# Kernel optimization log

Measured on AMD Instinct MI355X. Metric: run time of the kernel, lower is better.

The kernel has to match this reference:

```python
import jax, jax.numpy as jnp
import numpy as np

NX = 768
N_HEAD = 12
N_CTX = 2048
BATCH = 4
EPS = 1e-5
NEG = -1000000000.0


def _layernorm(x, g, b):
    # NOTE: faithful to source bug: returns g + normalized + b (additive, not scale)
    u = jnp.mean(x, axis=-1, keepdims=True)
    s = jnp.mean((x - u) ** 2, axis=-1, keepdims=True)
    return g + (x - u) / jnp.sqrt(s + EPS) + b


def setup_inputs() -> dict:
    key = jax.random.key(0)
    ks = jax.random.split(key, 8)
    std = 0.02
    x = jax.random.normal(ks[0], (BATCH, N_CTX, NX), dtype=jnp.float32)
    w_attn = jax.random.normal(ks[1], (NX, 3 * NX), dtype=jnp.float32) * std
    b_attn = jnp.zeros((3 * NX,), jnp.float32)
    w_proj = jax.random.normal(ks[2], (NX, NX), dtype=jnp.float32) * std
    b_proj = jnp.zeros((NX,), jnp.float32)
    ln1_g = jnp.ones((NX,), jnp.float32)
    ln1_b = jnp.zeros((NX,), jnp.float32)
    w_fc = jax.random.normal(ks[3], (NX, 4 * NX), dtype=jnp.float32) * std
    b_fc = jnp.zeros((4 * NX,), jnp.float32)
    w_fc2 = jax.random.normal(ks[4], (4 * NX, NX), dtype=jnp.float32) * std
    b_fc2 = jnp.zeros((NX,), jnp.float32)
    ln2_g = jnp.ones((NX,), jnp.float32)
    ln2_b = jnp.zeros((NX,), jnp.float32)
    return dict(x=x, w_attn=w_attn, b_attn=b_attn, w_proj=w_proj, b_proj=b_proj,
                ln1_g=ln1_g, ln1_b=ln1_b, w_fc=w_fc, b_fc=b_fc,
                w_fc2=w_fc2, b_fc2=b_fc2, ln2_g=ln2_g, ln2_b=ln2_b)


def reference(x, w_attn, b_attn, w_proj, b_proj, ln1_g, ln1_b,
              w_fc, b_fc, w_fc2, b_fc2, ln2_g, ln2_b):
    B, S, D = x.shape
    dh = D // N_HEAD
    # --- attention (scale=False: no 1/sqrt(d)) ---
    qkv = x @ w_attn + b_attn                      # [B,S,3D]
    q, k, v = jnp.split(qkv, 3, axis=-1)
    q = q.reshape(B, S, N_HEAD, dh).transpose(0, 2, 1, 3)   # [B,H,S,dh]
    k = k.reshape(B, S, N_HEAD, dh).transpose(0, 2, 3, 1)   # [B,H,dh,S]
    v = v.reshape(B, S, N_HEAD, dh).transpose(0, 2, 1, 3)   # [B,H,S,dh]
    w = jnp.einsum('bhsd,bhdt->bhst', q, k)        # [B,H,S,S]
    mask = jnp.tril(jnp.ones((S, S), x.dtype))[None, None]
    w = w * mask + NEG * (1.0 - mask)
    w = jax.nn.softmax(w, axis=-1)
    a = jnp.einsum('bhst,bhtd->bhsd', w, v)        # [B,H,S,dh]
    a = a.transpose(0, 2, 1, 3).reshape(B, S, D)
    a = a @ w_proj + b_proj
    # dropout layers are identity (eval mode)
    n = _layernorm(x + a, ln1_g, ln1_b)
    # --- MLP (intended ReLU; source's nn.ReLU usage is a bug) ---
    h = jax.nn.relu(n @ w_fc + b_fc)
    m = h @ w_fc2 + b_fc2
    return _layernorm(n + m, ln2_g, ln2_b)
```

## Files before the change

kernel.cpp:

```cpp
#include <hip/hip_runtime.h>
#include <stdint.h>

#define NX 768
#define SEQ 2048
#define NHEAD 12
#define MROWS 8192
#define LN_EPS 1e-5f
#define MASK_NEG -1000000000.0f

typedef __bf16 bf16x8 __attribute__((ext_vector_type(8)));
typedef float f32x4 __attribute__((ext_vector_type(4)));

#define AS3(p)  ((__attribute__((address_space(3))) void*)(p))
#define AS1C(p) ((const __attribute__((address_space(1))) void*)(p))

__device__ __forceinline__ unsigned short f2bf(float f) {
  union { float f; unsigned int u; } v; v.f = f;
  unsigned int r = v.u + 0x7fffu + ((v.u >> 16) & 1u);
  return (unsigned short)(r >> 16);
}
__device__ __forceinline__ unsigned int f2bf_fast_u(float f) {
  union { float f; unsigned int u; } v; v.f = f;
  return (v.u + 0x8000u) >> 16;
}
__device__ __forceinline__ float bf2f(unsigned short u) {
  union { unsigned int u; float f; } v; v.u = ((unsigned int)u) << 16;
  return v.f;
}

__global__ void convert_f32_bf16(const float* __restrict__ in,
                                 unsigned short* __restrict__ out, int n4) {
  int i = blockIdx.x * blockDim.x + threadIdx.x;
  if (i >= n4) return;
  float4 v = ((const float4*)in)[i];
  ushort4 o;
  o.x = f2bf(v.x); o.y = f2bf(v.y); o.z = f2bf(v.z); o.w = f2bf(v.w);
  ((ushort4*)out)[i] = o;
}

__global__ void transpose_w(const float* __restrict__ w,
                            unsigned short* __restrict__ wt, int K, int N) {
  __shared__ float tile[32][33];
  int n0 = blockIdx.x * 32, k0 = blockIdx.y * 32;
  int tx = threadIdx.x, ty = threadIdx.y;
#pragma unroll
  for (int j = 0; j < 4; ++j)
    tile[ty + j * 8][tx] = w[(long)(k0 + ty + j * 8) * N + n0 + tx];
  __syncthreads();
#pragma unroll
  for (int j = 0; j < 4; ++j)
    wt[(long)(n0 + ty + j * 8) * K + k0 + tx] = f2bf(tile[tx][ty + j * 8]);
}

__global__ void transpose_v(const unsigned short* __restrict__ qkv,
                            unsigned short* __restrict__ vt) {
  __shared__ unsigned short tile[64][68];
  int s0 = blockIdx.x * 64;
  int bh = blockIdx.y, b = bh / NHEAD, h = bh % NHEAD;
  int tx = threadIdx.x, ty = threadIdx.y;
  const unsigned short* src = qkv + (long)b * SEQ * 2304 + 1536 + h * 64;
#pragma unroll
  for (int j = 0; j < 4; ++j) {
    int s = ty + j * 16;
    ushort4 vv = *(const ushort4*)(src + (long)(s0 + s) * 2304 + tx * 4);
    *(ushort4*)(&tile[s][tx * 4]) = vv;
  }
  __syncthreads();
  unsigned short* dst = vt + (long)bh * 64 * SEQ + s0;
#pragma unroll
  for (int j = 0; j < 4; ++j) {
    int d = ty + j * 16;
    ushort4 o;
    o.x = tile[tx * 4 + 0][d]; o.y = tile[tx * 4 + 1][d];
    o.z = tile[tx * 4 + 2][d]; o.w = tile[tx * 4 + 3][d];
    *(ushort4*)(dst + (long)d * SEQ + tx * 4) = o;
  }
}

template <int ACT, int BN>
__global__ __launch_bounds__(256) void gemm_bt(const unsigned short* __restrict__ A,
                                               const unsigned short* __restrict__ Bt,
                                               const float* __restrict__ bias,
                                               unsigned short* __restrict__ C,
                                               int Nsz, int K) {
  __shared__ __align__(16) unsigned short smem[128 * 64 + BN * 64];
  unsigned short* As = smem;
  unsigned short* Bs = smem + 128 * 64;
  const int tid = threadIdx.x;
  const int w = tid >> 6, lane = tid & 63;
  const int l15 = lane & 15, quad = lane >> 4;
  constexpr int MT = (BN == 128) ? 4 : 2;
  const int wrow0 = (BN == 128) ? (w >> 1) * 64 : w * 32;
  const int wcol0 = (BN == 128) ? (w & 1) * 64 : 0;
  const long m0 = (long)blockIdx.y * 128;
  const long n0 = (long)blockIdx.x * BN;

  const int srow = tid >> 3;
  const int sg = tid & 7;

  f32x4 acc[MT][4] = {};

  for (int k0 = 0; k0 < K; k0 += 64) {
#pragma unroll
    for (int p = 0; p < 4; ++p) {
      int row = p * 32 + srow;
      int g = sg ^ (row & 7);
      const unsigned short* gA = A + (m0 + row) * (long)K + k0 + g * 8;
      __builtin_amdgcn_global_load_lds(AS1C(gA), AS3(As + p * 2048 + w * 512), 16, 0, 0);
    }
#pragma unroll
    for (int p = 0; p < BN / 32; ++p) {
      int row = p * 32 + srow;
      int g = sg ^ (row & 7);
      const unsigned short* gB = Bt + (n0 + row) * (long)K + k0 + g * 8;
      __builtin_amdgcn_global_load_lds(AS1C(gB), AS3(Bs + p * 2048 + w * 512), 16, 0, 0);
    }
    __syncthreads();

#pragma unroll
    for (int s2 = 0; s2 < 2; ++s2) {
      const int phys = ((s2 * 4 + quad) ^ (l15 & 7)) * 8;
      bf16x8 af[MT], bfr[4];
#pragma unroll
      for (int mt = 0; mt < MT; ++mt)
        af[mt] = *(const bf16x8*)(As + (wrow0 + mt * 16 + l15) * 64 + phys);
#pragma unroll
      for (int nt = 0; nt < 4; ++nt)
        bfr[nt] = *(const bf16x8*)(Bs + (wcol0 + nt * 16 + l15) * 64 + phys);
#pragma unroll
      for (int mt = 0; mt < MT; ++mt)
#pragma unroll
        for (int nt = 0; nt < 4; ++nt)
          acc[mt][nt] = __builtin_amdgcn_mfma_f32_16x16x32_bf16(af[mt], bfr[nt], acc[mt][nt], 0, 0, 0);
    }
    __syncthreads();
  }

  unsigned short* Ew = smem + w * (16 * 72);
  const long gmB = m0 + wrow0;
  const long gnB = n0 + wcol0;
  float bv[4];
#pragma unroll
  for (int nt = 0; nt < 4; ++nt) bv[nt] = bias[gnB + nt * 16 + l15];
  const int prow = lane >> 3, pcol = (lane & 7) * 8;
#pragma unroll
  for (int mt = 0; mt < MT; ++mt) {
#pragma unroll
    for (int nt = 0; nt < 4; ++nt)
#pragma unroll
      for (int r = 0; r < 4; ++r) {
        float v = acc[mt][nt][r] + bv[nt];
        if (ACT == 1) v = fmaxf(v, 0.f);
        Ew[(quad * 4 + r) * 72 + nt * 16 + l15] = f2bf(v);
      }
#pragma unroll
    for (int ps = 0; ps < 2; ++ps) {
      int row = ps * 8 + prow;
      int4 t = *(const int4*)(Ew + row * 72 + pcol);
      *(int4*)(C + (gmB + mt * 16 + row) * (long)Nsz + gnB + pcol) = t;
    }
  }
}

__global__ __launch_bounds__(256) void attn_v4(const unsigned short* __restrict__ qkv,
                                               const unsigned short* __restrict__ vt,
                                               unsigned short* __restrict__ out) {
  const int bx = blockIdx.x;
  const int bh = blockIdx.y;
  const int b = bh / NHEAD, h = bh % NHEAD;
  const int tid = threadIdx.x;
  const int w = tid >> 6, lane = tid & 63, l15 = lane & 15, quad = lane >> 4;

  __shared__ __align__(16) unsigned short Ks[128 * 64];
  __shared__ __align__(16) unsigned short Vs[64 * 128];
  __shared__ __align__(16) unsigned short Ps[4][16 * 128];

  const long rowbase = (long)b * SEQ;
  unsigned short* Pw = &Ps[w][0];
  const unsigned short* vbh = vt + (long)bh * 64 * SEQ;
  const float LOG2E = 1.4426950408889634f;

  const int krow = tid >> 3;
  const int kgo = (((tid & 7) ^ (krow & 7)) * 8);
  const int vd = tid >> 4;
  const int vgo = (((tid & 15) ^ vd) * 8);
  const unsigned short* kbase = qkv + rowbase * 2304L + 768 + h * 64;

  for (int pass = 0; pass < 2; ++pass) {
    const int qt = (pass == 0) ? bx : 31 - bx;
    const int nkeys = (qt + 1) * 64;
    const int qrow = qt * 64 + w * 16 + l15;
    const int qg = qt * 64 + w * 16 + l15;

    bf16x8 qf[2];
#pragma unroll
    for (int s2 = 0; s2 < 2; ++s2) {
      int4 raw = *(const int4*)(qkv + (rowbase + qrow) * 2304L + h * 64 + s2 * 32 + quad * 8);
      const unsigned short* rp = (const unsigned short*)&raw;
#pragma unroll
      for (int j = 0; j < 8; ++j)
        qf[s2][j] = (__bf16)(bf2f(rp[j]) * LOG2E);
    }

    const unsigned short* kp[4];
    const unsigned short* vp[4];
#pragma unroll
    for (int p = 0; p < 4; ++p) {
      kp[p] = kbase + (long)(p * 32 + krow) * 2304 + kgo;
      vp[p] = vbh + (long)(p * 16 + vd) * SEQ + vgo;
    }

    float l_sum = 0.f;
    f32x4 o_acc[4] = {};

    for (int k0 = 0; k0 < nkeys; k0 += 128) {
      __syncthreads();

#pragma unroll
      for (int p = 0; p < 4; ++p) {
        __builtin_amdgcn_global_load_lds(AS1C(kp[p]), AS3(Ks + p * 2048 + w * 512), 16, 0, 0);
        __builtin_amdgcn_global_load_lds(AS1C(vp[p]), AS3(Vs + p * 2048 + w * 512), 16, 0, 0);
        kp[p] += 128 * 2304;
        vp[p] += 128;
      }
      __syncthreads();

      f32x4 st[8];
#pragma unroll
      for (int nt = 0; nt < 8; ++nt) {
        f32x4 z = {};
        st[nt] = z;
        int key = nt * 16 + l15;
#pragma unroll
        for (int s2 = 0; s2 < 2; ++s2) {
          int phys = (s2 * 4 + quad) ^ (key & 7);
          bf16x8 kf = *(const bf16x8*)(Ks + key * 64 + phys * 8);
          st[nt] = __builtin_amdgcn_mfma_f32_16x16x32_bf16(kf, qf[s2], st[nt], 0, 0, 0);
        }
      }

      if (k0 + 128 > qt * 64) {
#pragma unroll
        for (int nt = 0; nt < 8; ++nt) {
          int kg = k0 + nt * 16 + quad * 4;
#pragma unroll
          for (int r = 0; r < 4; ++r)
            if (kg + r > qg) st[nt][r] = MASK_NEG;
        }
      }

      float psum = 0.f;
#pragma unroll
      for (int nt = 0; nt < 8; ++nt)
#pragma unroll
        for (int r = 0; r < 4; ++r) {
          float p = __builtin_amdgcn_exp2f(st[nt][r]);
          st[nt][r] = p;
          psum += p;
        }
      psum += __shfl_xor(psum, 16);
      psum += __shfl_xor(psum, 32);
      l_sum += psum;

#pragma unroll
      for (int nt = 0; nt < 8; ++nt) {
        unsigned int lo = f2bf_fast_u(st[nt][0]) | (f2bf_fast_u(st[nt][1]) << 16);
        unsigned int hi = f2bf_fast_u(st[nt][2]) | (f2bf_fast_u(st[nt][3]) << 16);
        int g16 = (nt * 2 + (quad >> 1)) ^ l15;
        uint2 pv; pv.x = lo; pv.y = hi;
        *(uint2*)(Pw + l15 * 128 + g16 * 8 + (quad & 1) * 4) = pv;
      }

#pragma unroll
      for (int c = 0; c < 4; ++c) {
        bf16x8 pf = *(const bf16x8*)(Pw + l15 * 128 + (((c * 4 + quad) ^ l15) * 8));
#pragma unroll
        for (int ntd = 0; ntd < 4; ++ntd) {
          int d = ntd * 16 + l15;
          int phys = (c * 4 + quad) ^ l15;
          bf16x8 vf = *(const bf16x8*)(Vs + d * 128 + phys * 8);
          o_acc[ntd] = __builtin_amdgcn_mfma_f32_16x16x32_bf16(pf, vf, o_acc[ntd], 0, 0, 0);
        }
      }
    }

#pragma unroll
    for (int r = 0; r < 4; ++r) {
      float lq = __shfl(l_sum, quad * 4 + r);
      float inv = 1.f / lq;
      int q = qt * 64 + w * 16 + quad * 4 + r;
#pragma unroll
      for (int ntd = 0; ntd < 4; ++ntd) {
        int d = ntd * 16 + l15;
        out[(rowbase + q) * (long)NX + h * 64 + d] = f2bf(o_acc[ntd][r] * inv);
      }
    }
  }
}

__global__ __launch_bounds__(256) void add_ln(const float* __restrict__ x_f,
                                              const unsigned short* __restrict__ x_b,
                                              const unsigned short* __restrict__ y_b,
                                              const float* __restrict__ g,
                                              const float* __restrict__ beta,
                                              float* __restrict__ out_f,
                                              unsigned short* __restrict__ out_b) {
  const int row = blockIdx.x, t = threadIdx.x;
  const long base = (long)row * NX;
  float v[3];
#pragma unroll
  for (int j = 0; j < 3; ++j) {
    int i = t + j * 256;
    float a = x_f ? x_f[base + i] : bf2f(x_b[base + i]);
    v[j] = a + bf2f(y_b[base + i]);
  }
  __shared__ float red[4];
  int wv = t >> 6, ln = t & 63;

  float ssum = v[0] + v[1] + v[2];
#pragma unroll
  for (int sh = 32; sh >= 1; sh >>= 1) ssum += __shfl_xor(ssum, sh);
  if (ln == 0) red[wv] = ssum;
  __syncthreads();
  float u = (red[0] + red[1] + red[2] + red[3]) * (1.f / NX);
  __syncthreads();

  float d0 = v[0] - u, d1 = v[1] - u, d2 = v[2] - u;
  float sq = d0 * d0 + d1 * d1 + d2 * d2;
#pragma unroll
  for (int sh = 32; sh >= 1; sh >>= 1) sq += __shfl_xor(sq, sh);
  if (ln == 0) red[wv] = sq;
  __syncthreads();
  float s = (red[0] + red[1] + red[2] + red[3]) * (1.f / NX);
  float rinv = rsqrtf(s + LN_EPS);

  float dd[3] = {d0, d1, d2};
#pragma unroll
  for (int j = 0; j < 3; ++j) {
    int i = t + j * 256;
    float o = g[i] + dd[j] * rinv + beta[i];
    if (out_f) out_f[base + i] = o;
    else out_b[base + i] = f2bf(o);
  }
}

extern "C" void kernel_launch(void* const* d_in, const int* in_sizes, int n_in,
                              void* d_out, int out_size, void* d_ws, size_t ws_size,
                              hipStream_t stream) {
  const float* x      = (const float*)d_in[0];
  const float* w_attn = (const float*)d_in[1];
  const float* b_attn = (const float*)d_in[2];
  const float* w_proj = (const float*)d_in[3];
  const float* b_proj = (const float*)d_in[4];
  const float* ln1_g  = (const float*)d_in[5];
  const float* ln1_b  = (const float*)d_in[6];
  const float* w_fc   = (const float*)d_in[7];
  const float* b_fc   = (const float*)d_in[8];
  const float* w_fc2  = (const float*)d_in[9];
  const float* b_fc2  = (const float*)d_in[10];
  const float* ln2_g  = (const float*)d_in[11];
  const float* ln2_b  = (const float*)d_in[12];
  float* out = (float*)d_out;

  char* ws = (char*)d_ws;
  size_t off = 0;
  auto alloc = [&](size_t bytes) {
    char* p = ws + off;
    off += (bytes + 255) & ~(size_t)255;
    return p;
  };
  unsigned short* xb      = (unsigned short*)alloc((size_t)MROWS * NX * 2);
  unsigned short* wt_attn = (unsigned short*)alloc((size_t)2304 * 768 * 2);
  unsigned short* wt_proj = (unsigned short*)alloc((size_t)768 * 768 * 2);
  unsigned short* wt_fc   = (unsigned short*)alloc((size_t)3072 * 768 * 2);
  unsigned short* wt_fc2  = (unsigned short*)alloc((size_t)768 * 3072 * 2);
  unsigned short* qkv     = (unsigned short*)alloc((size_t)MROWS * 3072 * 2);
  unsigned short* hbuf    = qkv;
  unsigned short* abuf    = (unsigned short*)alloc((size_t)MROWS * NX * 2);
  unsigned short* mbuf    = abuf;
  unsigned short* nbuf    = (unsigned short*)alloc((size_t)MROWS * NX * 2);
  unsigned short* vtb     = nbuf;
  unsigned short* pout    = xb;

  convert_f32_bf16<<<(MROWS * NX / 4 + 255) / 256, 256, 0, stream>>>(x, xb, MROWS * NX / 4);
  transpose_w<<<dim3(2304 / 32, 768 / 32), dim3(32, 8), 0, stream>>>(w_attn, wt_attn, 768, 2304);
  transpose_w<<<dim3(768 / 32, 768 / 32), dim3(32, 8), 0, stream>>>(w_proj, wt_proj, 768, 768);
  transpose_w<<<dim3(3072 / 32, 768 / 32), dim3(32, 8), 0, stream>>>(w_fc, wt_fc, 768, 3072);
  transpose_w<<<dim3(768 / 32, 3072 / 32), dim3(32, 8), 0, stream>>>(w_fc2, wt_fc2, 3072, 768);

  gemm_bt<0, 128><<<dim3(2304 / 128, MROWS / 128), 256, 0, stream>>>(xb, wt_attn, b_attn, qkv, 2304, 768);
  transpose_v<<<dim3(SEQ / 64, 48), dim3(16, 16), 0, stream>>>(qkv, vtb);
  attn_v4<<<dim3(16, 48), 256, 0, stream>>>(qkv, vtb, abuf);
  gemm_bt<0, 64><<<dim3(768 / 64, MROWS / 128), 256, 0, stream>>>(abuf, wt_proj, b_proj, pout, 768, 768);
  add_ln<<<MROWS, 256, 0, stream>>>(x, nullptr, pout, ln1_g, ln1_b, nullptr, nbuf);
  gemm_bt<1, 128><<<dim3(3072 / 128, MROWS / 128), 256, 0, stream>>>(nbuf, wt_fc, b_fc, hbuf, 3072, 768);
  gemm_bt<0, 64><<<dim3(768 / 64, MROWS / 128), 256, 0, stream>>>(hbuf, wt_fc2, b_fc2, mbuf, 768, 3072);
  add_ln<<<MROWS, 256, 0, stream>>>(nullptr, nbuf, mbuf, ln2_g, ln2_b, out, nullptr);
}
```

Before: 407.8 us.

## Double-buffer LDS tiles in GEMM and attention to overlap loads with MFMA

The GEMM kernel now uses two LDS buffers and issues the next K-tile's global_load_lds before computing on the current one, which also drops one barrier per iteration. The attention kernel is reworked to 64-key tiles with double-buffered K/V in LDS, prefetching the next tile while computing. Masking now applies only to the last tile, so masked work is less wasted. The trade is doubled GEMM shared memory, which may reduce occupancy, and twice as many attention iterations each with a barrier.

```diff
diff --git a/kernel.cpp b/kernel.cpp
--- a/kernel.cpp
+++ b/kernel.cpp
@@ -83,9 +83,10 @@
                                                const float* __restrict__ bias,
                                                unsigned short* __restrict__ C,
                                                int Nsz, int K) {
-  __shared__ __align__(16) unsigned short smem[128 * 64 + BN * 64];
-  unsigned short* As = smem;
-  unsigned short* Bs = smem + 128 * 64;
+  constexpr int ABUF = 128 * 64;
+  constexpr int BBUF = BN * 64;
+  constexpr int BUF = ABUF + BBUF;
+  __shared__ __align__(16) unsigned short smem[2 * BUF];
   const int tid = threadIdx.x;
   const int w = tid >> 6, lane = tid & 63;
   const int l15 = lane & 15, quad = lane >> 4;
@@ -98,9 +99,10 @@
   const int srow = tid >> 3;
   const int sg = tid & 7;
 
-  f32x4 acc[MT][4] = {};
-
-  for (int k0 = 0; k0 < K; k0 += 64) {
+  auto stage = [&](int kb) {
+    unsigned short* As = smem + (kb & 1) * BUF;
+    unsigned short* Bs = As + ABUF;
+    const int k0 = kb * 64;
 #pragma unroll
     for (int p = 0; p < 4; ++p) {
       int row = p * 32 + srow;
@@ -115,8 +117,17 @@
       const unsigned short* gB = Bt + (n0 + row) * (long)K + k0 + g * 8;
       __builtin_amdgcn_global_load_lds(AS1C(gB), AS3(Bs + p * 2048 + w * 512), 16, 0, 0);
     }
+  };
+
+  f32x4 acc[MT][4] = {};
+  const int nkb = K / 64;
+
+  stage(0);
+  for (int kb = 0; kb < nkb; ++kb) {
     __syncthreads();
-
+    if (kb + 1 < nkb) stage(kb + 1);
+    const unsigned short* As = smem + (kb & 1) * BUF;
+    const unsigned short* Bs = As + ABUF;
 #pragma unroll
     for (int s2 = 0; s2 < 2; ++s2) {
       const int phys = ((s2 * 4 + quad) ^ (l15 & 7)) * 8;
@@ -133,8 +144,8 @@
         for (int nt = 0; nt < 4; ++nt)
           acc[mt][nt] = __builtin_amdgcn_mfma_f32_16x16x32_bf16(af[mt], bfr[nt], acc[mt][nt], 0, 0, 0);
     }
-    __syncthreads();
-  }
+  }
+  __syncthreads();
 
   unsigned short* Ew = smem + w * (16 * 72);
   const long gmB = m0 + wrow0;
@@ -162,7 +173,7 @@
   }
 }
 
-__global__ __launch_bounds__(256) void attn_v4(const unsigned short* __restrict__ qkv,
+__global__ __launch_bounds__(256) void attn_v5(const unsigned short* __restrict__ qkv,
                                                const unsigned short* __restrict__ vt,
                                                unsigned short* __restrict__ out) {
   const int bx = blockIdx.x;
@@ -171,9 +182,9 @@
   const int tid = threadIdx.x;
   const int w = tid >> 6, lane = tid & 63, l15 = lane & 15, quad = lane >> 4;
 
-  __shared__ __align__(16) unsigned short Ks[128 * 64];
-  __shared__ __align__(16) unsigned short Vs[64 * 128];
-  __shared__ __align__(16) unsigned short Ps[4][16 * 128];
+  __shared__ __align__(16) unsigned short Ks[2][64 * 64];
+  __shared__ __align__(16) unsigned short Vs[2][64 * 64];
+  __shared__ __align__(16) unsigned short Ps[4][16 * 64];
 
   const long rowbase = (long)b * SEQ;
   unsigned short* Pw = &Ps[w][0];
@@ -182,15 +193,13 @@
 
   const int krow = tid >> 3;
   const int kgo = (((tid & 7) ^ (krow & 7)) * 8);
-  const int vd = tid >> 4;
-  const int vgo = (((tid & 15) ^ vd) * 8);
   const unsigned short* kbase = qkv + rowbase * 2304L + 768 + h * 64;
 
   for (int pass = 0; pass < 2; ++pass) {
     const int qt = (pass == 0) ? bx : 31 - bx;
-    const int nkeys = (qt + 1) * 64;
+    const int niter = qt + 1;
     const int qrow = qt * 64 + w * 16 + l15;
-    const int qg = qt * 64 + w * 16 + l15;
+    const int qg = qrow;
 
     bf16x8 qf[2];
 #pragma unroll
@@ -202,47 +211,57 @@
         qf[s2][j] = (__bf16)(bf2f(rp[j]) * LOG2E);
     }
 
-    const unsigned short* kp[4];
-    const unsigned short* vp[4];
-#pragma unroll
-    for (int p = 0; p < 4; ++p) {
+    const unsigned short* kp[2];
+    const unsigned short* vp[2];
+#pragma unroll
+    for (int p = 0; p < 2; ++p) {
       kp[p] = kbase + (long)(p * 32 + krow) * 2304 + kgo;
-      vp[p] = vbh + (long)(p * 16 + vd) * SEQ + vgo;
+      vp[p] = vbh + (long)(p * 32 + krow) * SEQ + kgo;
     }
 
     float l_sum = 0.f;
     f32x4 o_acc[4] = {};
 
-    for (int k0 = 0; k0 < nkeys; k0 += 128) {
+    __syncthreads();
+#pragma unroll
+    for (int p = 0; p < 2; ++p) {
+      __builtin_amdgcn_global_load_lds(AS1C(kp[p]), AS3(&Ks[0][0] + p * 2048 + w * 512), 16, 0, 0);
+      __builtin_amdgcn_global_load_lds(AS1C(vp[p]), AS3(&Vs[0][0] + p * 2048 + w * 512), 16, 0, 0);
+      kp[p] += 64 * 2304;
+      vp[p] += 64;
+    }
+
+    for (int it = 0; it < niter; ++it) {
       __syncthreads();
-
-#pragma unroll
-      for (int p = 0; p < 4; ++p) {
-        __builtin_amdgcn_global_load_lds(AS1C(kp[p]), AS3(Ks + p * 2048 + w * 512), 16, 0, 0);
-        __builtin_amdgcn_global_load_lds(AS1C(vp[p]), AS3(Vs + p * 2048 + w * 512), 16, 0, 0);
-        kp[p] += 128 * 2304;
-        vp[p] += 128;
-      }
-      __syncthreads();
-
-      f32x4 st[8];
-#pragma unroll
-      for (int nt = 0; nt < 8; ++nt) {
-        f32x4 z = {};
-        st[nt] = z;
+      if (it + 1 < niter) {
+        const int nb = (it + 1) & 1;
+#pragma unroll
+        for (int p = 0; p < 2; ++p) {
+          __builtin_amdgcn_global_load_lds(AS1C(kp[p]), AS3(&Ks[nb][0] + p * 2048 + w * 512), 16, 0, 0);
+          __builtin_amdgcn_global_load_lds(AS1C(vp[p]), AS3(&Vs[nb][0] + p * 2048 + w * 512), 16, 0, 0);
+          kp[p] += 64 * 2304;
+          vp[p] += 64;
+        }
+      }
+      const unsigned short* Kc = &Ks[it & 1][0];
+      const unsigned short* Vc = &Vs[it & 1][0];
+
+      f32x4 st[4] = {};
+#pragma unroll
+      for (int nt = 0; nt < 4; ++nt) {
         int key = nt * 16 + l15;
 #pragma unroll
         for (int s2 = 0; s2 < 2; ++s2) {
           int phys = (s2 * 4 + quad) ^ (key & 7);
-          bf16x8 kf = *(const bf16x8*)(Ks + key * 64 + phys * 8);
+          bf16x8 kf = *(const bf16x8*)(Kc + key * 64 + phys * 8);
           st[nt] = __builtin_amdgcn_mfma_f32_16x16x32_bf16(kf, qf[s2], st[nt], 0, 0, 0);
         }
       }
 
-      if (k0 + 128 > qt * 64) {
-#pragma unroll
-        for (int nt = 0; nt < 8; ++nt) {
-          int kg = k0 + nt * 16 + quad * 4;
+      if (it == niter - 1) {
+#pragma unroll
+        for (int nt = 0; nt < 4; ++nt) {
+          int kg = it * 64 + nt * 16 + quad * 4;
 #pragma unroll
           for (int r = 0; r < 4; ++r)
             if (kg + r > qg) st[nt][r] = MASK_NEG;
@@ -251,7 +270,7 @@
 
       float psum = 0.f;
 #pragma unroll
-      for (int nt = 0; nt < 8; ++nt)
+      for (int nt = 0; nt < 4; ++nt)
 #pragma unroll
         for (int r = 0; r < 4; ++r) {
           float p = __builtin_amdgcn_exp2f(st[nt][r]);
@@ -263,22 +282,22 @@
       l_sum += psum;
 
 #pragma unroll
-      for (int nt = 0; nt < 8; ++nt) {
+      for (int nt = 0; nt < 4; ++nt) {
         unsigned int lo = f2bf_fast_u(st[nt][0]) | (f2bf_fast_u(st[nt][1]) << 16);
         unsigned int hi = f2bf_fast_u(st[nt][2]) | (f2bf_fast_u(st[nt][3]) << 16);
-        int g16 = (nt * 2 + (quad >> 1)) ^ l15;
+        int g8 = (nt * 2 + (quad >> 1)) ^ (l15 & 7);
         uint2 pv; pv.x = lo; pv.y = hi;
-        *(uint2*)(Pw + l15 * 128 + g16 * 8 + (quad & 1) * 4) = pv;
-      }
-
-#pragma unroll
-      for (int c = 0; c < 4; ++c) {
-        bf16x8 pf = *(const bf16x8*)(Pw + l15 * 128 + (((c * 4 + quad) ^ l15) * 8));
+        *(uint2*)(Pw + l15 * 64 + g8 * 8 + (quad & 1) * 4) = pv;
+      }
+
+#pragma unroll
+      for (int c = 0; c < 2; ++c) {
+        int phys = ((c * 4 + quad) ^ (l15 & 7)) * 8;
+        bf16x8 pf = *(const bf16x8*)(Pw + l15 * 64 + phys);
 #pragma unroll
         for (int ntd = 0; ntd < 4; ++ntd) {
           int d = ntd * 16 + l15;
-          int phys = (c * 4 + quad) ^ l15;
-          bf16x8 vf = *(const bf16x8*)(Vs + d * 128 + phys * 8);
+          bf16x8 vf = *(const bf16x8*)(Vc + d * 64 + phys);
           o_acc[ntd] = __builtin_amdgcn_mfma_f32_16x16x32_bf16(pf, vf, o_acc[ntd], 0, 0, 0);
         }
       }
@@ -390,7 +409,7 @@
 
   gemm_bt<0, 128><<<dim3(2304 / 128, MROWS / 128), 256, 0, stream>>>(xb, wt_attn, b_attn, qkv, 2304, 768);
   transpose_v<<<dim3(SEQ / 64, 48), dim3(16, 16), 0, stream>>>(qkv, vtb);
-  attn_v4<<<dim3(16, 48), 256, 0, stream>>>(qkv, vtb, abuf);
+  attn_v5<<<dim3(16, 48), 256, 0, stream>>>(qkv, vtb, abuf);
   gemm_bt<0, 64><<<dim3(768 / 64, MROWS / 128), 256, 0, stream>>>(abuf, wt_proj, b_proj, pout, 768, 768);
   add_ln<<<MROWS, 256, 0, stream>>>(x, nullptr, pout, ln1_g, ln1_b, nullptr, nbuf);
   gemm_bt<1, 128><<<dim3(3072 / 128, MROWS / 128), 256, 0, stream>>>(nbuf, wt_fc, b_fc, hbuf, 3072, 768);
```

New measurement: 385.8 us. 1.06x faster.
